# Performance work log

Measured on AMD Instinct MI355X. Metric: run time of the kernel, lower is better.

## Reference

```python
import jax, jax.numpy as jnp
import numpy as np
import math

D_MODEL = 1024
NUM_HEADS = 16
BATCH = 2
SEQ = 2048

def setup_inputs() -> dict:
    key = jax.random.key(0)
    ks = jax.random.split(key, 9)
    s = 1.0 / math.sqrt(D_MODEL)
    inp = {
        "X": jax.random.normal(ks[0], (BATCH, SEQ, D_MODEL), dtype=jnp.float32),
        "Wq": jax.random.uniform(ks[1], (D_MODEL, D_MODEL), jnp.float32, -s, s),
        "bq": jax.random.uniform(ks[2], (D_MODEL,), jnp.float32, -s, s),
        "Wk": jax.random.uniform(ks[3], (D_MODEL, D_MODEL), jnp.float32, -s, s),
        "bk": jax.random.uniform(ks[4], (D_MODEL,), jnp.float32, -s, s),
        "Wv": jax.random.uniform(ks[5], (D_MODEL, D_MODEL), jnp.float32, -s, s),
        "bv": jax.random.uniform(ks[6], (D_MODEL,), jnp.float32, -s, s),
        "Wo": jax.random.uniform(ks[7], (D_MODEL, D_MODEL), jnp.float32, -s, s),
        "bo": jax.random.uniform(ks[8], (D_MODEL,), jnp.float32, -s, s),
    }
    return inp

def reference(X, Wq, bq, Wk, bk, Wv, bv, Wo, bo):
    B, S, D = X.shape
    H = NUM_HEADS
    dk = D // H
    # QKV projections (Linear: x @ W.T + b; here W stored as [in, out] so x @ W + b)
    q = X @ Wq + bq
    k = X @ Wk + bk
    v = X @ Wv + bv
    # split heads -> [B, H, S, dk]
    q = q.reshape(B, S, H, dk).transpose(0, 2, 1, 3)
    k = k.reshape(B, S, H, dk).transpose(0, 2, 1, 3)
    v = v.reshape(B, S, H, dk).transpose(0, 2, 1, 3)
    scores = jnp.einsum("bhqd,bhkd->bhqk", q, k) / math.sqrt(dk)
    weights = jax.nn.softmax(scores, axis=-1)
    attn = jnp.einsum("bhqk,bhkd->bhqd", weights, v)
    concat = attn.transpose(0, 2, 1, 3).reshape(B, S, D)
    return concat @ Wo + bo
```

## Files before the change

kernel.cpp:

```cpp
#include <hip/hip_runtime.h>
#include <stdint.h>

#define D_MODEL 1024
#define NH      16
#define DKH     64
#define BATCH   2
#define SEQ     2048
#define M_TOK   (BATCH*SEQ)

typedef __attribute__((ext_vector_type(8))) short bf16x8;
typedef __attribute__((ext_vector_type(4))) float f32x4;

__device__ __forceinline__ uint16_t f2b(float f) {
  uint32_t u = __builtin_bit_cast(uint32_t, f);
  return (uint16_t)((u + 0x7FFFu + ((u >> 16) & 1u)) >> 16);
}

__device__ __forceinline__ void gl2lds16(const uint16_t* g, uint16_t* l) {
  __builtin_amdgcn_global_load_lds(
      (const __attribute__((address_space(1))) void*)g,
      (__attribute__((address_space(3))) void*)l, 16, 0, 0);
}

__global__ __launch_bounds__(256) void prep(
    const float* __restrict__ X, uint16_t* __restrict__ Xb,
    const float* __restrict__ W0, const float* __restrict__ W1,
    const float* __restrict__ W2, const float* __restrict__ W3,
    uint16_t* __restrict__ T0, uint16_t* __restrict__ T1,
    uint16_t* __restrict__ T2, uint16_t* __restrict__ T3) {
  const int bid = blockIdx.x;
  if (bid < 2048) {
    int i = (bid * 256 + threadIdx.x) * 8;
    float4 a = *(const float4*)(X + i);
    float4 b = *(const float4*)(X + i + 4);
    uint16_t tmp[8] = {f2b(a.x), f2b(a.y), f2b(a.z), f2b(a.w),
                       f2b(b.x), f2b(b.y), f2b(b.z), f2b(b.w)};
    *(uint4*)(Xb + i) = *(const uint4*)tmp;
  } else {
    __shared__ float tile[32][33];
    int r = bid - 2048;
    int z = r >> 10, tt = r & 1023;
    const float* W = (z == 0) ? W0 : (z == 1) ? W1 : (z == 2) ? W2 : W3;
    uint16_t*    T = (z == 0) ? T0 : (z == 1) ? T1 : (z == 2) ? T2 : T3;
    int k0 = (tt & 31) * 32, n0 = (tt >> 5) * 32;
    int t = threadIdx.x;
    int rr = t >> 3, c4 = (t & 7) * 4;
    float4 v = *(const float4*)(W + (size_t)(k0 + rr) * D_MODEL + n0 + c4);
    tile[rr][c4] = v.x; tile[rr][c4 + 1] = v.y;
    tile[rr][c4 + 2] = v.z; tile[rr][c4 + 3] = v.w;
    __syncthreads();
    uint16_t o[4] = {f2b(tile[c4][rr]), f2b(tile[c4 + 1][rr]),
                     f2b(tile[c4 + 2][rr]), f2b(tile[c4 + 3][rr])};
    *(uint2*)(T + (size_t)(n0 + rr) * D_MODEL + k0 + c4) = *(const uint2*)o;
  }
}

template <bool SWAP>
__device__ __forceinline__ void gemm_core(const uint16_t* __restrict__ A,
                                          const uint16_t* __restrict__ BT,
                                          uint16_t* As, uint16_t* Bs,
                                          int m0, int n0, int kBeg, int kEnd,
                                          f32x4 (&acc)[4][4]) {
  const int t    = threadIdx.x;
  const int lane = t & 63;
  const int qi   = lane & 15, g = lane >> 4;
  const int wm   = (t >> 7) & 1;
  const int wn   = (t >> 6) & 1;
  const int srow = t >> 2;
  const int sc   = (t & 3) ^ ((t >> 3) & 3);
  const int wbase = t & 192;
  const int rch  = (g ^ ((qi >> 1) & 3)) * 8;

  const uint16_t* Ag = A  + (size_t)(m0 + srow) * D_MODEL + sc * 8;
  const uint16_t* Bg = BT + (size_t)(n0 + srow) * D_MODEL + sc * 8;

#pragma unroll
  for (int j = 0; j < 2; j++) {
    gl2lds16(Ag + (size_t)j * 64 * D_MODEL + kBeg, As + (j * 256 + wbase) * 8);
    gl2lds16(Bg + (size_t)j * 64 * D_MODEL + kBeg, Bs + (j * 256 + wbase) * 8);
  }

  int cur = 0;
  for (int k0 = kBeg; k0 < kEnd; k0 += 32) {
    __syncthreads();
    int kn = k0 + 32;
    if (kn < kEnd) {
      int nb = (cur ^ 1) * 4096;
#pragma unroll
      for (int j = 0; j < 2; j++) {
        gl2lds16(Ag + (size_t)j * 64 * D_MODEL + kn, As + nb + (j * 256 + wbase) * 8);
        gl2lds16(Bg + (size_t)j * 64 * D_MODEL + kn, Bs + nb + (j * 256 + wbase) * 8);
      }
    }
    const uint16_t* Ab = As + cur * 4096;
    const uint16_t* Bb = Bs + cur * 4096;
    bf16x8 af[4], bf[4];
#pragma unroll
    for (int i = 0; i < 4; i++) {
      af[i] = *(const bf16x8*)(Ab + (wm * 64 + i * 16 + qi) * 32 + rch);
      bf[i] = *(const bf16x8*)(Bb + (wn * 64 + i * 16 + qi) * 32 + rch);
    }
#pragma unroll
    for (int i = 0; i < 4; i++)
#pragma unroll
      for (int j = 0; j < 4; j++)
        acc[i][j] = SWAP
          ? __builtin_amdgcn_mfma_f32_16x16x32_bf16(bf[j], af[i], acc[i][j], 0, 0, 0)
          : __builtin_amdgcn_mfma_f32_16x16x32_bf16(af[i], bf[j], acc[i][j], 0, 0, 0);
    cur ^= 1;
  }
}

__global__ __launch_bounds__(256) void qkv_gemm(
    const uint16_t* __restrict__ Xb,
    const uint16_t* __restrict__ WqT, const uint16_t* __restrict__ WkT,
    const uint16_t* __restrict__ WvT,
    const float* __restrict__ bq, const float* __restrict__ bk,
    const float* __restrict__ bv,
    uint16_t* __restrict__ Qo, uint16_t* __restrict__ Ko, uint16_t* __restrict__ Vt) {
  __shared__ __align__(16) uint16_t smem[17408];
  uint16_t* As = smem;
  uint16_t* Bs = smem + 8192;
  uint16_t* T  = smem;
  const int z = blockIdx.z;
  const uint16_t* BT  = (z == 0) ? WqT : (z == 1) ? WkT : WvT;
  const float*   bias = (z == 0) ? bq  : (z == 1) ? bk  : bv;
  const int m0 = blockIdx.y * 128, n0 = blockIdx.x * 128;
  const int lane = threadIdx.x & 63, qi = lane & 15, g = lane >> 4;
  const int wm = (threadIdx.x >> 7) & 1, wn = (threadIdx.x >> 6) & 1;
  const float l2e = 1.4426950408889634f * 0.125f;

  const f32x4 ZERO = {0.f, 0.f, 0.f, 0.f};
  f32x4 acc[4][4];
#pragma unroll
  for (int i = 0; i < 4; i++)
#pragma unroll
    for (int j = 0; j < 4; j++) acc[i][j] = ZERO;

  if (z == 2) {
    gemm_core<false>(Xb, BT, As, Bs, m0, n0, 0, D_MODEL, acc);
    __syncthreads();
#pragma unroll
    for (int i = 0; i < 4; i++) {
      int tok = wm * 64 + i * 16 + g * 4;
#pragma unroll
      for (int j = 0; j < 4; j++) {
        int ch = wn * 64 + j * 16 + qi;
        float bb = bias[n0 + ch];
        uint32_t lo = (uint32_t)f2b(acc[i][j][0] + bb) | ((uint32_t)f2b(acc[i][j][1] + bb) << 16);
        uint32_t hi = (uint32_t)f2b(acc[i][j][2] + bb) | ((uint32_t)f2b(acc[i][j][3] + bb) << 16);
        uint2 pk = {lo, hi};
        *(uint2*)(T + ch * 136 + tok) = pk;
      }
    }
    __syncthreads();
    {
      int ch = threadIdx.x >> 1, sh = threadIdx.x & 1;
      const uint16_t* src = T + ch * 136 + sh * 64;
      int bidx = m0 >> 11;
      uint16_t* dst = Vt + ((size_t)(bidx * D_MODEL + n0 + ch)) * SEQ + (m0 & 2047) + sh * 64;
#pragma unroll
      for (int u = 0; u < 8; u++)
        *(uint4*)(dst + u * 8) = *(const uint4*)(src + u * 8);
    }
  } else {
    gemm_core<true>(Xb, BT, As, Bs, m0, n0, 0, D_MODEL, acc);
    uint16_t* O = z ? Ko : Qo;
    const float osc = (z == 0) ? l2e : 1.0f;
#pragma unroll
    for (int i = 0; i < 4; i++) {
      size_t tok = m0 + wm * 64 + i * 16 + qi;
#pragma unroll
      for (int j = 0; j < 4; j++) {
        int ch = n0 + wn * 64 + j * 16 + g * 4;
        float4 bb = *(const float4*)(bias + ch);
        uint32_t lo = (uint32_t)f2b((acc[i][j][0] + bb.x) * osc) |
                      ((uint32_t)f2b((acc[i][j][1] + bb.y) * osc) << 16);
        uint32_t hi = (uint32_t)f2b((acc[i][j][2] + bb.z) * osc) |
                      ((uint32_t)f2b((acc[i][j][3] + bb.w) * osc) << 16);
        uint2 pk = {lo, hi};
        *(uint2*)(O + tok * D_MODEL + ch) = pk;
      }
    }
  }
}

__global__ __launch_bounds__(256) void oproj_gemm(
    const uint16_t* __restrict__ Ab, const uint16_t* __restrict__ WoT,
    const float* __restrict__ bo, float* __restrict__ out) {
  __shared__ __align__(16) uint16_t smem[16384];
  uint16_t* As = smem;
  uint16_t* Bs = smem + 8192;
  const int lane = threadIdx.x & 63, qi = lane & 15, g = lane >> 4;
  const int wm = (threadIdx.x >> 7) & 1, wn = (threadIdx.x >> 6) & 1;
  const int m0 = blockIdx.y * 128, n0 = blockIdx.x * 128;

  const f32x4 ZERO = {0.f, 0.f, 0.f, 0.f};
  f32x4 acc[4][4];
#pragma unroll
  for (int i = 0; i < 4; i++)
#pragma unroll
    for (int j = 0; j < 4; j++) acc[i][j] = ZERO;

  gemm_core<true>(Ab, WoT, As, Bs, m0, n0, 0, D_MODEL, acc);

#pragma unroll
  for (int i = 0; i < 4; i++) {
    size_t tok = m0 + wm * 64 + i * 16 + qi;
#pragma unroll
    for (int j = 0; j < 4; j++) {
      int ch = n0 + wn * 64 + j * 16 + g * 4;
      float4 bb = *(const float4*)(bo + ch);
      float4 o = {acc[i][j][0] + bb.x, acc[i][j][1] + bb.y,
                  acc[i][j][2] + bb.z, acc[i][j][3] + bb.w};
      *(float4*)(out + tok * D_MODEL + ch) = o;
    }
  }
}

__global__ __launch_bounds__(512, 2) void attn_fwd(
    const uint16_t* __restrict__ Q, const uint16_t* __restrict__ K,
    const uint16_t* __restrict__ Vt, uint16_t* __restrict__ O) {
  __shared__ __align__(16) uint16_t sm[36864];
  uint16_t* const Ps = sm + 20480;

  const int t = threadIdx.x, lane = t & 63, w = t >> 6;
  const int g = lane >> 4, qi = lane & 15;
  const int rch = (g ^ ((qi >> 1) & 3)) * 8;
  const int key = qi & 7;
  const int q0 = blockIdx.y * 256;
  const int bh = blockIdx.x, b = bh >> 4, h = bh & 15;
  const uint16_t* Qp = Q + (size_t)b * SEQ * D_MODEL + h * DKH;
  const uint16_t* Kp = K + (size_t)b * SEQ * D_MODEL + h * DKH;
  const uint16_t* Vp = Vt + (size_t)bh * DKH * SEQ;

  const int tt = t & 255, hs = t >> 8;
  const int srow = tt >> 2;
  const int sc = (tt & 3) ^ ((tt >> 3) & 3);
  const int wbase = tt & 192;

  bf16x8 qf[2][2];
#pragma unroll
  for (int i = 0; i < 2; i++) {
    const uint16_t* Qr = Qp + (size_t)(q0 + w * 32 + i * 16 + qi) * D_MODEL + g * 8;
    qf[0][i] = *(const bf16x8*)(Qr);
    qf[1][i] = *(const bf16x8*)(Qr + 32);
  }

  auto STAGE = [&](int tile, uint16_t* kb, uint16_t* vb) {
    gl2lds16(Kp + (size_t)(tile * 64 + srow) * D_MODEL + hs * 32 + sc * 8,
             kb + hs * 2048 + wbase * 8);
    gl2lds16(Vp + (size_t)srow * SEQ + tile * 64 + hs * 32 + sc * 8,
             vb + hs * 2048 + wbase * 8);
  };

  float lsum[2] = {0.f, 0.f};
  const f32x4 ZERO = {0.f, 0.f, 0.f, 0.f};
  f32x4 oaccT[4][2];
#pragma unroll
  for (int d = 0; d < 4; d++)
#pragma unroll
    for (int i = 0; i < 2; i++) oaccT[d][i] = ZERO;

  auto QK_SM = [&](const uint16_t* Kb) {
    f32x4 sacc[4][2];
#pragma unroll
    for (int j = 0; j < 4; j++)
#pragma unroll
      for (int i = 0; i < 2; i++) sacc[j][i] = ZERO;
#pragma unroll
    for (int ks = 0; ks < 2; ks++) {
      const uint16_t* Ksb = Kb + ks * 2048;
      bf16x8 kf[4];
#pragma unroll
      for (int j = 0; j < 4; j++)
        kf[j] = *(const bf16x8*)(Ksb + (j * 16 + qi) * 32 + rch);
      __builtin_amdgcn_s_setprio(1);
#pragma unroll
      for (int j = 0; j < 4; j++)
#pragma unroll
        for (int i = 0; i < 2; i++)
          sacc[j][i] = __builtin_amdgcn_mfma_f32_16x16x32_bf16(kf[j], qf[ks][i], sacc[j][i], 0, 0, 0);
      __builtin_amdgcn_s_setprio(0);
    }
#pragma unroll
    for (int i = 0; i < 2; i++) {
      uint16_t* Pr = Ps + (w * 32 + i * 16 + qi) * 64;
#pragma unroll
      for (int j = 0; j < 4; j++) {
        float p0 = __builtin_amdgcn_exp2f(sacc[j][i][0]);
        float p1 = __builtin_amdgcn_exp2f(sacc[j][i][1]);
        float p2 = __builtin_amdgcn_exp2f(sacc[j][i][2]);
        float p3 = __builtin_amdgcn_exp2f(sacc[j][i][3]);
        lsum[i] += (p0 + p1) + (p2 + p3);
        uint2 pk = {__builtin_amdgcn_perm(__builtin_bit_cast(uint32_t, p1),
                                          __builtin_bit_cast(uint32_t, p0), 0x07060302u),
                    __builtin_amdgcn_perm(__builtin_bit_cast(uint32_t, p3),
                                          __builtin_bit_cast(uint32_t, p2), 0x07060302u)};
        *(uint2*)(Pr + (((j * 4 + g) ^ (2 * key)) << 2)) = pk;
      }
    }
  };

  auto PV = [&](const uint16_t* Vb) {
#pragma unroll
    for (int ks = 0; ks < 2; ks++) {
      const uint16_t* Vsb = Vb + ks * 2048;
      bf16x8 vf[4], pf[2];
#pragma unroll
      for (int d = 0; d < 4; d++)
        vf[d] = *(const bf16x8*)(Vsb + (d * 16 + qi) * 32 + rch);
#pragma unroll
      for (int i = 0; i < 2; i++)
        pf[i] = *(const bf16x8*)(Ps + (w * 32 + i * 16 + qi) * 64 +
                                 (((ks * 4 + g) ^ key) << 3));
      __builtin_amdgcn_s_setprio(1);
#pragma unroll
      for (int d = 0; d < 4; d++)
#pragma unroll
        for (int i = 0; i < 2; i++)
          oaccT[d][i] = __builtin_amdgcn_mfma_f32_16x16x32_bf16(vf[d], pf[i], oaccT[d][i], 0, 0, 0);
      __builtin_amdgcn_s_setprio(0);
    }
  };

  STAGE(0, sm, sm + 8192);
  STAGE(1, sm + 4096, sm + 8192 + 4096);
  __syncthreads();
  QK_SM(sm);
  __syncthreads();

  for (int kt = 1; kt < SEQ / 64; kt++) {
    if (kt + 1 < SEQ / 64)
      STAGE(kt + 1, sm + ((kt + 1) & 1) * 4096,
            sm + 8192 + ((kt + 1) % 3) * 4096);
    const uint16_t* Kb = sm + (kt & 1) * 4096;
    const uint16_t* Vb = sm + 8192 + ((kt - 1) % 3) * 4096;
    PV(Vb);
    QK_SM(Kb);
    if (kt + 1 < SEQ / 64) __syncthreads();
  }
  PV(sm + 8192 + ((SEQ / 64 - 1) % 3) * 4096);

#pragma unroll
  for (int i = 0; i < 2; i++) {
    lsum[i] += __shfl_xor(lsum[i], 16, 64);
    lsum[i] += __shfl_xor(lsum[i], 32, 64);
  }
  float rl[2] = {1.f / lsum[0], 1.f / lsum[1]};

#pragma unroll
  for (int i = 0; i < 2; i++) {
    size_t row = (size_t)b * SEQ + q0 + w * 32 + i * 16 + qi;
#pragma unroll
    for (int d = 0; d < 4; d++) {
      uint32_t lo = (uint32_t)f2b(oaccT[d][i][0] * rl[i]) |
                    ((uint32_t)f2b(oaccT[d][i][1] * rl[i]) << 16);
      uint32_t hi = (uint32_t)f2b(oaccT[d][i][2] * rl[i]) |
                    ((uint32_t)f2b(oaccT[d][i][3] * rl[i]) << 16);
      uint2 pk = {lo, hi};
      *(uint2*)(O + row * D_MODEL + h * DKH + d * 16 + g * 4) = pk;
    }
  }
}

extern "C" void kernel_launch(void* const* d_in, const int* in_sizes, int n_in,
                              void* d_out, int out_size, void* d_ws, size_t ws_size,
                              hipStream_t stream) {
  (void)in_sizes; (void)n_in; (void)out_size; (void)ws_size;
  const float* X  = (const float*)d_in[0];
  const float* Wq = (const float*)d_in[1];
  const float* bq = (const float*)d_in[2];
  const float* Wk = (const float*)d_in[3];
  const float* bk = (const float*)d_in[4];
  const float* Wv = (const float*)d_in[5];
  const float* bv = (const float*)d_in[6];
  const float* Wo = (const float*)d_in[7];
  const float* bo = (const float*)d_in[8];
  float* out = (float*)d_out;

  char* p = (char*)d_ws;
  uint16_t* Xb  = (uint16_t*)p; p += (size_t)M_TOK * D_MODEL * 2;
  uint16_t* WqT = (uint16_t*)p; p += (size_t)D_MODEL * D_MODEL * 2;
  uint16_t* WkT = (uint16_t*)p; p += (size_t)D_MODEL * D_MODEL * 2;
  uint16_t* WvT = (uint16_t*)p; p += (size_t)D_MODEL * D_MODEL * 2;
  uint16_t* WoT = (uint16_t*)p; p += (size_t)D_MODEL * D_MODEL * 2;
  uint16_t* Qw  = (uint16_t*)p; p += (size_t)M_TOK * D_MODEL * 2;
  uint16_t* Kw  = (uint16_t*)p; p += (size_t)M_TOK * D_MODEL * 2;
  uint16_t* Vt  = (uint16_t*)p; p += (size_t)M_TOK * D_MODEL * 2;
  uint16_t* Ob  = (uint16_t*)p; p += (size_t)M_TOK * D_MODEL * 2;

  prep<<<6144, 256, 0, stream>>>(X, Xb, Wq, Wk, Wv, Wo, WqT, WkT, WvT, WoT);
  qkv_gemm<<<dim3(8, 32, 3), 256, 0, stream>>>(Xb, WqT, WkT, WvT, bq, bk, bv, Qw, Kw, Vt);
  attn_fwd<<<dim3(BATCH * NH, SEQ / 256), 512, 0, stream>>>(Qw, Kw, Vt, Ob);
  oproj_gemm<<<dim3(8, 32), 256, 0, stream>>>(Ob, WoT, bo, out);
}
```

Baseline: 184.4 us.

## Deepen attention K/V pipeline to four stages and remap QKV GEMM blocks

The attention kernel now gives K and V four LDS ring slots each, prefetching three tiles ahead with an explicit vmcnt wait plus barrier instead of full __syncthreads. QK and PV run on the same tile each iteration, which removes the skewed prologue and epilogue. The QKV GEMM switches to a 1D grid with a swizzled block-to-tile mapping for better L2 reuse, and adds a 3-blocks-per-CU occupancy hint. The extra LDS in attention (96KB per block) may limit occupancy, and the clamped redundant prefetches at the tail add some wasted loads.

```diff
diff --git a/kernel.cpp b/kernel.cpp
--- a/kernel.cpp
+++ b/kernel.cpp
@@ -111,7 +111,7 @@
   }
 }
 
-__global__ __launch_bounds__(256) void qkv_gemm(
+__global__ __launch_bounds__(256, 3) void qkv_gemm(
     const uint16_t* __restrict__ Xb,
     const uint16_t* __restrict__ WqT, const uint16_t* __restrict__ WkT,
     const uint16_t* __restrict__ WvT,
@@ -122,10 +122,12 @@
   uint16_t* As = smem;
   uint16_t* Bs = smem + 8192;
   uint16_t* T  = smem;
-  const int z = blockIdx.z;
+  const int bid = blockIdx.x;
+  const int xg = bid & 7, nn = (bid >> 3) & 7, mloc = (bid >> 6) & 3;
+  const int z = bid >> 8;
   const uint16_t* BT  = (z == 0) ? WqT : (z == 1) ? WkT : WvT;
   const float*   bias = (z == 0) ? bq  : (z == 1) ? bk  : bv;
-  const int m0 = blockIdx.y * 128, n0 = blockIdx.x * 128;
+  const int m0 = (xg * 4 + mloc) * 128, n0 = nn * 128;
   const int lane = threadIdx.x & 63, qi = lane & 15, g = lane >> 4;
   const int wm = (threadIdx.x >> 7) & 1, wn = (threadIdx.x >> 6) & 1;
   const float l2e = 1.4426950408889634f * 0.125f;
@@ -221,8 +223,8 @@
 __global__ __launch_bounds__(512, 2) void attn_fwd(
     const uint16_t* __restrict__ Q, const uint16_t* __restrict__ K,
     const uint16_t* __restrict__ Vt, uint16_t* __restrict__ O) {
-  __shared__ __align__(16) uint16_t sm[36864];
-  uint16_t* const Ps = sm + 20480;
+  __shared__ __align__(16) uint16_t sm[49152];
+  uint16_t* const Ps = sm + 32768;
 
   const int t = threadIdx.x, lane = t & 63, w = t >> 6;
   const int g = lane >> 4, qi = lane & 15;
@@ -247,11 +249,11 @@
     qf[1][i] = *(const bf16x8*)(Qr + 32);
   }
 
-  auto STAGE = [&](int tile, uint16_t* kb, uint16_t* vb) {
+  auto STAGE = [&](int tile, int slot) {
     gl2lds16(Kp + (size_t)(tile * 64 + srow) * D_MODEL + hs * 32 + sc * 8,
-             kb + hs * 2048 + wbase * 8);
+             sm + slot * 4096 + hs * 2048 + wbase * 8);
     gl2lds16(Vp + (size_t)srow * SEQ + tile * 64 + hs * 32 + sc * 8,
-             vb + hs * 2048 + wbase * 8);
+             sm + 16384 + slot * 4096 + hs * 2048 + wbase * 8);
   };
 
   float lsum[2] = {0.f, 0.f};
@@ -324,23 +326,23 @@
     }
   };
 
-  STAGE(0, sm, sm + 8192);
-  STAGE(1, sm + 4096, sm + 8192 + 4096);
-  __syncthreads();
-  QK_SM(sm);
-  __syncthreads();
-
-  for (int kt = 1; kt < SEQ / 64; kt++) {
-    if (kt + 1 < SEQ / 64)
-      STAGE(kt + 1, sm + ((kt + 1) & 1) * 4096,
-            sm + 8192 + ((kt + 1) % 3) * 4096);
-    const uint16_t* Kb = sm + (kt & 1) * 4096;
-    const uint16_t* Vb = sm + 8192 + ((kt - 1) % 3) * 4096;
+  STAGE(0, 0); STAGE(1, 1); STAGE(2, 2);
+  asm volatile("s_waitcnt vmcnt(4)" ::: "memory");
+  __builtin_amdgcn_s_barrier();
+  asm volatile("" ::: "memory");
+
+  for (int kt = 0; kt < SEQ / 64; kt++) {
+    int st = kt + 3;
+    if (st > SEQ / 64 - 1) st = SEQ / 64 - 1;
+    STAGE(st, (kt + 3) & 3);
+    const uint16_t* Kb = sm + (kt & 3) * 4096;
+    const uint16_t* Vb = sm + 16384 + (kt & 3) * 4096;
+    QK_SM(Kb);
     PV(Vb);
-    QK_SM(Kb);
-    if (kt + 1 < SEQ / 64) __syncthreads();
-  }
-  PV(sm + 8192 + ((SEQ / 64 - 1) % 3) * 4096);
+    asm volatile("s_waitcnt vmcnt(4)" ::: "memory");
+    __builtin_amdgcn_s_barrier();
+    asm volatile("" ::: "memory");
+  }
 
 #pragma unroll
   for (int i = 0; i < 2; i++) {
@@ -391,7 +393,7 @@
   uint16_t* Ob  = (uint16_t*)p; p += (size_t)M_TOK * D_MODEL * 2;
 
   prep<<<6144, 256, 0, stream>>>(X, Xb, Wq, Wk, Wv, Wo, WqT, WkT, WvT, WoT);
-  qkv_gemm<<<dim3(8, 32, 3), 256, 0, stream>>>(Xb, WqT, WkT, WvT, bq, bk, bv, Qw, Kw, Vt);
+  qkv_gemm<<<768, 256, 0, stream>>>(Xb, WqT, WkT, WvT, bq, bk, bv, Qw, Kw, Vt);
   attn_fwd<<<dim3(BATCH * NH, SEQ / 256), 512, 0, stream>>>(Qw, Kw, Vt, Ob);
   oproj_gemm<<<dim3(8, 32), 256, 0, stream>>>(Ob, WoT, bo, out);
 }
```

After: 183.7 us. Within noise of the previous version (-0.4%).
